# Kernel optimization log

Hardware: AMD Instinct MI355X
Metric: run time of the kernel (lower is better)

Reference implementation:

```python
import jax, jax.numpy as jnp
import numpy as np


def setup_inputs() -> dict:
    key = jax.random.key(0)
    n_class, n_support, n_query, feature_dim = 32, 16, 16, 1024
    n_rows = n_class * n_support + n_query * n_class  # 1024
    data = jax.random.normal(key, (n_rows, feature_dim), dtype=jnp.float32)
    return {"data": data, "n_class": n_class, "n_support": n_support, "n_query": n_query}


def reference(data, n_class, n_support, n_query):
    D = data.shape[-1]
    # support: [n_class, n_support, D]; query: [n_query*n_class, D]
    support = data[: n_class * n_support].reshape(n_class, n_support, D)
    query = data[n_class * n_support :]
    # attention score: tanh(elementwise product) summed over feature dim
    # scores: [Q, n_class, n_support]  (Q = n_query*n_class)
    scores = jnp.tanh(support[None, :, :, :] * query[:, None, None, :]).sum(-1)
    att = jax.nn.softmax(scores, axis=-1)  # softmax over n_support
    # weighted instance pooling -> prototypes per (query, class): [Q, n_class, D]
    proto = jnp.einsum("qcs,csd->qcd", att, support)
    return proto
```

## Files before the change

kernel.cpp:

```cpp
#include <hip/hip_runtime.h>

constexpr int NC = 32, NS = 16, NQ = 512, D = 1024;
constexpr int QPB = 8;

__global__ __launch_bounds__(256, 2)
void proto_attn_kernel(const float* __restrict__ data, float* __restrict__ out) {
    const int c    = blockIdx.x;
    const int qt   = blockIdx.y;
    const int tid  = threadIdx.x;
    const int wave = tid >> 6;
    const int lane = tid & 63;

    __shared__ float4 sup4[NS * (D / 4)];

    const float4* sg = reinterpret_cast<const float4*>(data + (size_t)c * NS * D);
    #pragma unroll
    for (int i = 0; i < 16; ++i)
        sup4[tid + 256 * i] = sg[tid + 256 * i];
    __syncthreads();

    const float K = 2.88539008177792681472f;
    const int q0 = qt * QPB + wave * 2;
    float4 qa[4], qb[4];
    const float4* qg0 = reinterpret_cast<const float4*>(data + (size_t)(NC * NS + q0) * D);
    const float4* qg1 = reinterpret_cast<const float4*>(data + (size_t)(NC * NS + q0 + 1) * D);
    #pragma unroll
    for (int j = 0; j < 4; ++j) {
        float4 t0 = qg0[lane + 64 * j];
        float4 t1 = qg1[lane + 64 * j];
        qa[j] = make_float4(t0.x * K, t0.y * K, t0.z * K, t0.w * K);
        qb[j] = make_float4(t1.x * K, t1.y * K, t1.z * K, t1.w * K);
    }

    float sc0[NS], sc1[NS];
    #pragma unroll
    for (int s = 0; s < NS; ++s) {
        float r0 = 0.f, r1 = 0.f;
        #pragma unroll
        for (int j = 0; j < 4; ++j) {
            float4 sv = sup4[s * (D / 4) + lane + 64 * j];
            r0 += __builtin_amdgcn_rcpf(__builtin_amdgcn_exp2f(sv.x * qa[j].x) + 1.f);
            r0 += __builtin_amdgcn_rcpf(__builtin_amdgcn_exp2f(sv.y * qa[j].y) + 1.f);
            r0 += __builtin_amdgcn_rcpf(__builtin_amdgcn_exp2f(sv.z * qa[j].z) + 1.f);
            r0 += __builtin_amdgcn_rcpf(__builtin_amdgcn_exp2f(sv.w * qa[j].w) + 1.f);
            r1 += __builtin_amdgcn_rcpf(__builtin_amdgcn_exp2f(sv.x * qb[j].x) + 1.f);
            r1 += __builtin_amdgcn_rcpf(__builtin_amdgcn_exp2f(sv.y * qb[j].y) + 1.f);
            r1 += __builtin_amdgcn_rcpf(__builtin_amdgcn_exp2f(sv.z * qb[j].z) + 1.f);
            r1 += __builtin_amdgcn_rcpf(__builtin_amdgcn_exp2f(sv.w * qb[j].w) + 1.f);
        }
        #pragma unroll
        for (int m = 32; m >= 1; m >>= 1) {
            r0 += __shfl_xor(r0, m, 64);
            r1 += __shfl_xor(r1, m, 64);
        }
        sc0[s] = (float)D - 2.f * r0;
        sc1[s] = (float)D - 2.f * r1;
    }

    const float L2E = 1.44269504088896340736f;
    float m0 = sc0[0], m1 = sc1[0];
    #pragma unroll
    for (int s = 1; s < NS; ++s) { m0 = fmaxf(m0, sc0[s]); m1 = fmaxf(m1, sc1[s]); }
    float sum0 = 0.f, sum1 = 0.f;
    #pragma unroll
    for (int s = 0; s < NS; ++s) {
        sc0[s] = __builtin_amdgcn_exp2f((sc0[s] - m0) * L2E);
        sc1[s] = __builtin_amdgcn_exp2f((sc1[s] - m1) * L2E);
        sum0 += sc0[s];
        sum1 += sc1[s];
    }
    const float inv0 = __builtin_amdgcn_rcpf(sum0);
    const float inv1 = __builtin_amdgcn_rcpf(sum1);

    float4 o0[4], o1[4];
    #pragma unroll
    for (int j = 0; j < 4; ++j) {
        o0[j] = make_float4(0.f, 0.f, 0.f, 0.f);
        o1[j] = make_float4(0.f, 0.f, 0.f, 0.f);
    }
    #pragma unroll
    for (int s = 0; s < NS; ++s) {
        const float a0 = sc0[s] * inv0;
        const float a1 = sc1[s] * inv1;
        #pragma unroll
        for (int j = 0; j < 4; ++j) {
            float4 sv = sup4[s * (D / 4) + lane + 64 * j];
            o0[j].x += a0 * sv.x; o0[j].y += a0 * sv.y;
            o0[j].z += a0 * sv.z; o0[j].w += a0 * sv.w;
            o1[j].x += a1 * sv.x; o1[j].y += a1 * sv.y;
            o1[j].z += a1 * sv.z; o1[j].w += a1 * sv.w;
        }
    }
    float4* og0 = reinterpret_cast<float4*>(out + ((size_t)q0 * NC + c) * D);
    float4* og1 = reinterpret_cast<float4*>(out + ((size_t)(q0 + 1) * NC + c) * D);
    #pragma unroll
    for (int j = 0; j < 4; ++j) {
        og0[lane + 64 * j] = o0[j];
        og1[lane + 64 * j] = o1[j];
    }
}

extern "C" void kernel_launch(void* const* d_in, const int* in_sizes, int n_in,
                              void* d_out, int out_size, void* d_ws, size_t ws_size,
                              hipStream_t stream) {
    (void)in_sizes; (void)n_in; (void)out_size; (void)d_ws; (void)ws_size;
    const float* data = (const float*)d_in[0];
    float* out = (float*)d_out;
    dim3 grid(NC, NQ / QPB);
    proto_attn_kernel<<<grid, dim3(256), 0, stream>>>(data, out);
}
```

Measured before the change: 154.5 us.

## Read support straight from global, four queries per wave, nontemporal stores

After: 187.3 us. 21.2% more time.

```diff
diff --git a/kernel.cpp b/kernel.cpp
--- a/kernel.cpp
+++ b/kernel.cpp
@@ -1,9 +1,13 @@
 #include <hip/hip_runtime.h>
 
 constexpr int NC = 32, NS = 16, NQ = 512, D = 1024;
-constexpr int QPB = 8;
+constexpr int QPW = 4;
+constexpr int WPB = 4;
+constexpr int QPB = QPW * WPB;
 
-__global__ __launch_bounds__(256, 2)
+typedef float vfloat4 __attribute__((ext_vector_type(4)));
+
+__global__ __launch_bounds__(256)
 void proto_attn_kernel(const float* __restrict__ data, float* __restrict__ out) {
     const int c    = blockIdx.x;
     const int qt   = blockIdx.y;
@@ -11,92 +15,95 @@
     const int wave = tid >> 6;
     const int lane = tid & 63;
 
-    __shared__ float4 sup4[NS * (D / 4)];
+    const float Kc  = 2.88539008177792681472f;
+    const float L2E = 1.44269504088896340736f;
 
-    const float4* sg = reinterpret_cast<const float4*>(data + (size_t)c * NS * D);
+    const int q0 = qt * QPB + wave * QPW;
+
+    vfloat4 q[QPW][4];
     #pragma unroll
-    for (int i = 0; i < 16; ++i)
-        sup4[tid + 256 * i] = sg[tid + 256 * i];
-    __syncthreads();
-
-    const float K = 2.88539008177792681472f;
-    const int q0 = qt * QPB + wave * 2;
-    float4 qa[4], qb[4];
-    const float4* qg0 = reinterpret_cast<const float4*>(data + (size_t)(NC * NS + q0) * D);
-    const float4* qg1 = reinterpret_cast<const float4*>(data + (size_t)(NC * NS + q0 + 1) * D);
-    #pragma unroll
-    for (int j = 0; j < 4; ++j) {
-        float4 t0 = qg0[lane + 64 * j];
-        float4 t1 = qg1[lane + 64 * j];
-        qa[j] = make_float4(t0.x * K, t0.y * K, t0.z * K, t0.w * K);
-        qb[j] = make_float4(t1.x * K, t1.y * K, t1.z * K, t1.w * K);
+    for (int qi = 0; qi < QPW; ++qi) {
+        const vfloat4* qg = reinterpret_cast<const vfloat4*>(
+            data + (size_t)(NC * NS + q0 + qi) * D);
+        #pragma unroll
+        for (int j = 0; j < 4; ++j) {
+            vfloat4 t = qg[lane + 64 * j];
+            q[qi][j] = t * Kc;
+        }
     }
 
-    float sc0[NS], sc1[NS];
-    #pragma unroll
+    const vfloat4* sup = reinterpret_cast<const vfloat4*>(data + (size_t)c * NS * D);
+
+    float sc[QPW][NS];
+    #pragma unroll 4
     for (int s = 0; s < NS; ++s) {
-        float r0 = 0.f, r1 = 0.f;
+        float r[QPW] = {0.f, 0.f, 0.f, 0.f};
         #pragma unroll
         for (int j = 0; j < 4; ++j) {
-            float4 sv = sup4[s * (D / 4) + lane + 64 * j];
-            r0 += __builtin_amdgcn_rcpf(__builtin_amdgcn_exp2f(sv.x * qa[j].x) + 1.f);
-            r0 += __builtin_amdgcn_rcpf(__builtin_amdgcn_exp2f(sv.y * qa[j].y) + 1.f);
-            r0 += __builtin_amdgcn_rcpf(__builtin_amdgcn_exp2f(sv.z * qa[j].z) + 1.f);
-            r0 += __builtin_amdgcn_rcpf(__builtin_amdgcn_exp2f(sv.w * qa[j].w) + 1.f);
-            r1 += __builtin_amdgcn_rcpf(__builtin_amdgcn_exp2f(sv.x * qb[j].x) + 1.f);
-            r1 += __builtin_amdgcn_rcpf(__builtin_amdgcn_exp2f(sv.y * qb[j].y) + 1.f);
-            r1 += __builtin_amdgcn_rcpf(__builtin_amdgcn_exp2f(sv.z * qb[j].z) + 1.f);
-            r1 += __builtin_amdgcn_rcpf(__builtin_amdgcn_exp2f(sv.w * qb[j].w) + 1.f);
+            const vfloat4 sv = sup[s * (D / 4) + lane + 64 * j];
+            #pragma unroll
+            for (int qi = 0; qi < QPW; ++qi) {
+                r[qi] += __builtin_amdgcn_rcpf(__builtin_amdgcn_exp2f(sv.x * q[qi][j].x) + 1.f);
+                r[qi] += __builtin_amdgcn_rcpf(__builtin_amdgcn_exp2f(sv.y * q[qi][j].y) + 1.f);
+                r[qi] += __builtin_amdgcn_rcpf(__builtin_amdgcn_exp2f(sv.z * q[qi][j].z) + 1.f);
+                r[qi] += __builtin_amdgcn_rcpf(__builtin_amdgcn_exp2f(sv.w * q[qi][j].w) + 1.f);
+            }
         }
         #pragma unroll
         for (int m = 32; m >= 1; m >>= 1) {
-            r0 += __shfl_xor(r0, m, 64);
-            r1 += __shfl_xor(r1, m, 64);
+            #pragma unroll
+            for (int qi = 0; qi < QPW; ++qi)
+                r[qi] += __shfl_xor(r[qi], m, 64);
         }
-        sc0[s] = (float)D - 2.f * r0;
-        sc1[s] = (float)D - 2.f * r1;
+        #pragma unroll
+        for (int qi = 0; qi < QPW; ++qi)
+            sc[qi][s] = (float)D - 2.f * r[qi];
     }
 
-    const float L2E = 1.44269504088896340736f;
-    float m0 = sc0[0], m1 = sc1[0];
     #pragma unroll
-    for (int s = 1; s < NS; ++s) { m0 = fmaxf(m0, sc0[s]); m1 = fmaxf(m1, sc1[s]); }
-    float sum0 = 0.f, sum1 = 0.f;
+    for (int qi = 0; qi < QPW; ++qi) {
+        float m = sc[qi][0];
+        #pragma unroll
+        for (int s = 1; s < NS; ++s) m = fmaxf(m, sc[qi][s]);
+        float sum = 0.f;
+        #pragma unroll
+        for (int s = 0; s < NS; ++s) {
+            sc[qi][s] = __builtin_amdgcn_exp2f((sc[qi][s] - m) * L2E);
+            sum += sc[qi][s];
+        }
+        const float inv = __builtin_amdgcn_rcpf(sum);
+        #pragma unroll
+        for (int s = 0; s < NS; ++s) sc[qi][s] *= inv;
+    }
+
+    vfloat4 acc[QPW][4];
     #pragma unroll
+    for (int qi = 0; qi < QPW; ++qi)
+        #pragma unroll
+        for (int j = 0; j < 4; ++j)
+            acc[qi][j] = (vfloat4)(0.f);
+
+    #pragma unroll 4
     for (int s = 0; s < NS; ++s) {
-        sc0[s] = __builtin_amdgcn_exp2f((sc0[s] - m0) * L2E);
-        sc1[s] = __builtin_amdgcn_exp2f((sc1[s] - m1) * L2E);
-        sum0 += sc0[s];
-        sum1 += sc1[s];
-    }
-    const float inv0 = __builtin_amdgcn_rcpf(sum0);
-    const float inv1 = __builtin_amdgcn_rcpf(sum1);
-
-    float4 o0[4], o1[4];
-    #pragma unroll
-    for (int j = 0; j < 4; ++j) {
-        o0[j] = make_float4(0.f, 0.f, 0.f, 0.f);
-        o1[j] = make_float4(0.f, 0.f, 0.f, 0.f);
-    }
-    #pragma unroll
-    for (int s = 0; s < NS; ++s) {
-        const float a0 = sc0[s] * inv0;
-        const float a1 = sc1[s] * inv1;
         #pragma unroll
         for (int j = 0; j < 4; ++j) {
-            float4 sv = sup4[s * (D / 4) + lane + 64 * j];
-            o0[j].x += a0 * sv.x; o0[j].y += a0 * sv.y;
-            o0[j].z += a0 * sv.z; o0[j].w += a0 * sv.w;
-            o1[j].x += a1 * sv.x; o1[j].y += a1 * sv.y;
-            o1[j].z += a1 * sv.z; o1[j].w += a1 * sv.w;
+            const vfloat4 sv = sup[s * (D / 4) + lane + 64 * j];
+            #pragma unroll
+            for (int qi = 0; qi < QPW; ++qi) {
+                acc[qi][j].x = fmaf(sc[qi][s], sv.x, acc[qi][j].x);
+                acc[qi][j].y = fmaf(sc[qi][s], sv.y, acc[qi][j].y);
+                acc[qi][j].z = fmaf(sc[qi][s], sv.z, acc[qi][j].z);
+                acc[qi][j].w = fmaf(sc[qi][s], sv.w, acc[qi][j].w);
+            }
         }
     }
-    float4* og0 = reinterpret_cast<float4*>(out + ((size_t)q0 * NC + c) * D);
-    float4* og1 = reinterpret_cast<float4*>(out + ((size_t)(q0 + 1) * NC + c) * D);
+
     #pragma unroll
-    for (int j = 0; j < 4; ++j) {
-        og0[lane + 64 * j] = o0[j];
-        og1[lane + 64 * j] = o1[j];
+    for (int qi = 0; qi < QPW; ++qi) {
+        vfloat4* og = reinterpret_cast<vfloat4*>(out + ((size_t)(q0 + qi) * NC + c) * D);
+        #pragma unroll
+        for (int j = 0; j < 4; ++j)
+            __builtin_nontemporal_store(acc[qi][j], og + lane + 64 * j);
     }
 }
 
```
